# Kernel optimization log

Hardware: AMD Instinct MI355X
Metric: run time of the kernel (lower is better)

The kernel has to match this reference:

```python
import jax, jax.numpy as jnp
import numpy as np

S, B, D, H = 2048, 2, 1024, 16
DK = D // H  # 64

def setup_inputs() -> dict:
    key = jax.random.key(0)
    ks = jax.random.split(key, 11)
    scale = 1.0 / np.sqrt(D)
    return {
        "query": jax.random.normal(ks[0], (S, B, D), dtype=jnp.float32),
        "key":   jax.random.normal(ks[1], (S, B, D), dtype=jnp.float32),
        "value": jax.random.normal(ks[2], (S, B, D), dtype=jnp.float32),
        "Wq": jax.random.normal(ks[3], (D, D), dtype=jnp.float32) * scale,
        "bq": jax.random.normal(ks[4], (D,), dtype=jnp.float32) * scale,
        "Wk": jax.random.normal(ks[5], (D, D), dtype=jnp.float32) * scale,
        "bk": jax.random.normal(ks[6], (D,), dtype=jnp.float32) * scale,
        "Wv": jax.random.normal(ks[7], (D, D), dtype=jnp.float32) * scale,
        "bv": jax.random.normal(ks[8], (D,), dtype=jnp.float32) * scale,
        "Wo": jax.random.normal(ks[9], (D, D), dtype=jnp.float32) * scale,
        "bo": jax.random.normal(ks[10], (D,), dtype=jnp.float32) * scale,
    }

def _split_heads(x):
    # [S, B, D] -> [H, B, S, DK]  (matches .view(S,B,H,DK).transpose(0,2))
    return x.reshape(S, B, H, DK).transpose(2, 1, 0, 3)

def reference(query, key, value, Wq, bq, Wk, bk, Wv, bv, Wo, bo):
    q = _split_heads(query @ Wq.T + bq)
    k = _split_heads(key   @ Wk.T + bk)
    v = _split_heads(value @ Wv.T + bv)
    scores = jnp.einsum('hbqd,hbkd->hbqk', q, k) / jnp.sqrt(jnp.float32(DK))
    align = jax.nn.softmax(scores, axis=-1)
    x = jnp.einsum('hbqk,hbkd->hbqd', align, v)  # [H,B,S,DK]
    x = x.transpose(2, 1, 0, 3).reshape(S, B, D)  # back to [S,B,D]
    return x @ Wo.T + bo
```

## Files before the change

### kernel.cpp

```cpp
#include <hip/hip_runtime.h>
#include <math.h>

#define SS 2048
#define BB 2
#define DD 1024
#define HH 16
#define DKK 64
#define MM (SS*BB)

typedef _Float16 f16;
typedef __attribute__((ext_vector_type(8))) _Float16 f16x8;
typedef __attribute__((ext_vector_type(2))) __fp16 fp16x2r;
typedef __attribute__((ext_vector_type(4))) float f32x4;
typedef __attribute__((ext_vector_type(16))) float f32x16;

__device__ __forceinline__ unsigned pk2(float a, float b) {
    union { fp16x2r h; unsigned u; } v;
    v.h = __builtin_amdgcn_cvt_pkrtz(a, b);
    return v.u;
}
__device__ __forceinline__ void gload_lds16(const void* g, void* l) {
    __builtin_amdgcn_global_load_lds(
        (const __attribute__((address_space(1))) unsigned*)g,
        (__attribute__((address_space(3))) unsigned*)l, 16, 0, 0);
}

__global__ __launch_bounds__(256)
void cvt_x(const float* __restrict__ q, const float* __restrict__ k,
           const float* __restrict__ v, f16* __restrict__ out)
{
    const int z = blockIdx.y;
    const float* src = z == 0 ? q : (z == 1 ? k : v);
    size_t t = (size_t)blockIdx.x*256 + threadIdx.x;
    float4 f0 = ((const float4*)src)[t*2];
    float4 f1 = ((const float4*)src)[t*2+1];
    uint4 r;
    r.x = pk2(f0.x, f0.y); r.y = pk2(f0.z, f0.w);
    r.z = pk2(f1.x, f1.y); r.w = pk2(f1.z, f1.w);
    ((uint4*)(out + (size_t)z*MM*DD))[t] = r;
}

__global__ __launch_bounds__(256)
void cvt_w(const float* __restrict__ wq, const float* __restrict__ wk,
           const float* __restrict__ wv, const float* __restrict__ wo,
           f16* __restrict__ out)
{
    const int z = blockIdx.y;
    const float* src = z == 0 ? wq : (z == 1 ? wk : (z == 2 ? wv : wo));
    size_t t = (size_t)blockIdx.x*256 + threadIdx.x;
    float4 f0 = ((const float4*)src)[t*2];
    float4 f1 = ((const float4*)src)[t*2+1];
    uint4 r;
    r.x = pk2(f0.x, f0.y); r.y = pk2(f0.z, f0.w);
    r.z = pk2(f1.x, f1.y); r.w = pk2(f1.z, f1.w);
    ((uint4*)(out + (size_t)z*DD*DD))[t] = r;
}

__global__ __launch_bounds__(256)
void qkv_gemm(const f16* __restrict__ A16, const f16* __restrict__ W16,
              const float* __restrict__ bq, const float* __restrict__ bk,
              const float* __restrict__ bv,
              f16* __restrict__ Qh, f16* __restrict__ Kh, f16* __restrict__ Vt)
{
    __shared__ __align__(16) f16 As[128*32];
    __shared__ __align__(16) f16 Bs[128*32];

    const int tid  = threadIdx.x;
    const int w    = tid >> 6;
    const int lane = tid & 63;
    const int ln   = lane & 15;
    const int quad = lane >> 4;
    const int z  = blockIdx.z;
    const int m0 = blockIdx.x * 128;
    const int n0 = blockIdx.y * 128;
    const int wm = (w >> 1) * 64;
    const int wn = (w & 1) * 64;

    const f16* A = A16 + (size_t)z*MM*DD;
    const f16* W = W16 + (size_t)z*DD*DD;
    const float* bias = z == 0 ? bq : (z == 1 ? bk : bv);

    f32x4 acc[4][4];
    #pragma unroll
    for (int mt = 0; mt < 4; mt++)
        #pragma unroll
        for (int nt = 0; nt < 4; nt++)
            acc[mt][nt] = (f32x4){0.f,0.f,0.f,0.f};

    int slot[2], r_[2], gch[2];
    #pragma unroll
    for (int i = 0; i < 2; i++) {
        slot[i] = i*256 + tid;
        r_[i]   = slot[i] >> 2;
        gch[i]  = ((slot[i] & 3) ^ ((r_[i] >> 1) & 3)) * 8;
    }

    for (int step = 0; step < DD/32; step++) {
        const int k0 = step*32;
        __syncthreads();
        #pragma unroll
        for (int i = 0; i < 2; i++) {
            gload_lds16(A + (size_t)(m0 + r_[i])*DD + k0 + gch[i],
                        (char*)As + slot[i]*16);
            gload_lds16(W + (size_t)(n0 + r_[i])*DD + k0 + gch[i],
                        (char*)Bs + slot[i]*16);
        }
        __syncthreads();

        f16x8 af[4], bf[4];
        #pragma unroll
        for (int mt = 0; mt < 4; mt++) {
            int r = wm + mt*16 + ln;
            af[mt] = *(const f16x8*)&As[r*32 + ((quad ^ ((r>>1)&3)) << 3)];
        }
        #pragma unroll
        for (int nt = 0; nt < 4; nt++) {
            int r = wn + nt*16 + ln;
            bf[nt] = *(const f16x8*)&Bs[r*32 + ((quad ^ ((r>>1)&3)) << 3)];
        }
        #pragma unroll
        for (int mt = 0; mt < 4; mt++)
            #pragma unroll
            for (int nt = 0; nt < 4; nt++)
                acc[mt][nt] = __builtin_amdgcn_mfma_f32_16x16x32_f16(
                    af[mt], bf[nt], acc[mt][nt], 0, 0, 0);
    }

    float bvv[4];
    #pragma unroll
    for (int nt = 0; nt < 4; nt++) bvv[nt] = bias[n0 + wn + nt*16 + ln];

    if (z == 2) {
        #pragma unroll
        for (int mt = 0; mt < 4; mt++) {
            int mbase = m0 + wm + mt*16 + quad*4;
            int s0 = mbase >> 1;
            #pragma unroll
            for (int nt = 0; nt < 4; nt++) {
                int n = n0 + wn + nt*16 + ln;
                int h = n >> 6, d = n & 63;
                float v0 = acc[mt][nt][0] + bvv[nt];
                float v1 = acc[mt][nt][1] + bvv[nt];
                float v2 = acc[mt][nt][2] + bvv[nt];
                float v3 = acc[mt][nt][3] + bvv[nt];
                *(unsigned*)&Vt[((size_t)(0*HH + h)*DKK + d)*SS + s0] = pk2(v0, v2);
                *(unsigned*)&Vt[((size_t)(1*HH + h)*DKK + d)*SS + s0] = pk2(v1, v3);
            }
        }
    } else {
        const float scale = z == 0 ? 0.125f : 1.0f;
        f16* dst = z == 0 ? Qh : Kh;
        #pragma unroll
        for (int mt = 0; mt < 4; mt++)
            #pragma unroll
            for (int nt = 0; nt < 4; nt++)
                #pragma unroll
                for (int r = 0; r < 4; r++) {
                    int m = m0 + wm + mt*16 + quad*4 + r;
                    int n = n0 + wn + nt*16 + ln;
                    int s = m >> 1, b = m & 1;
                    int h = n >> 6, d = n & 63;
                    dst[(((size_t)(b*HH + h))*SS + s)*DKK + d] =
                        (f16)((acc[mt][nt][r] + bvv[nt]) * scale);
                }
    }
}

__global__ __launch_bounds__(256)
void out_gemm(const f16* __restrict__ A, const f16* __restrict__ W,
              const float* __restrict__ bias, float* __restrict__ out)
{
    __shared__ __align__(16) f16 As[64*32];
    __shared__ __align__(16) f16 Bs[128*32];

    const int tid  = threadIdx.x;
    const int w    = tid >> 6;
    const int lane = tid & 63;
    const int ln   = lane & 15;
    const int quad = lane >> 4;
    const int m0 = blockIdx.x * 64;
    const int n0 = blockIdx.y * 128;
    const int wm = (w >> 1) * 32;
    const int wn = (w & 1) * 64;

    f32x4 acc[2][4];
    #pragma unroll
    for (int mt = 0; mt < 2; mt++)
        #pragma unroll
        for (int nt = 0; nt < 4; nt++)
            acc[mt][nt] = (f32x4){0.f,0.f,0.f,0.f};

    const int rA  = tid >> 2;
    const int gchA = ((tid & 3) ^ ((rA >> 1) & 3)) * 8;
    int slotB[2], rB[2], gchB[2];
    #pragma unroll
    for (int i = 0; i < 2; i++) {
        slotB[i] = i*256 + tid;
        rB[i]    = slotB[i] >> 2;
        gchB[i]  = ((slotB[i] & 3) ^ ((rB[i] >> 1) & 3)) * 8;
    }

    for (int step = 0; step < DD/32; step++) {
        const int k0 = step*32;
        __syncthreads();
        gload_lds16(A + (size_t)(m0 + rA)*DD + k0 + gchA, (char*)As + tid*16);
        #pragma unroll
        for (int i = 0; i < 2; i++)
            gload_lds16(W + (size_t)(n0 + rB[i])*DD + k0 + gchB[i],
                        (char*)Bs + slotB[i]*16);
        __syncthreads();

        f16x8 af[2], bf[4];
        #pragma unroll
        for (int mt = 0; mt < 2; mt++) {
            int r = wm + mt*16 + ln;
            af[mt] = *(const f16x8*)&As[r*32 + ((quad ^ ((r>>1)&3)) << 3)];
        }
        #pragma unroll
        for (int nt = 0; nt < 4; nt++) {
            int r = wn + nt*16 + ln;
            bf[nt] = *(const f16x8*)&Bs[r*32 + ((quad ^ ((r>>1)&3)) << 3)];
        }
        #pragma unroll
        for (int mt = 0; mt < 2; mt++)
            #pragma unroll
            for (int nt = 0; nt < 4; nt++)
                acc[mt][nt] = __builtin_amdgcn_mfma_f32_16x16x32_f16(
                    af[mt], bf[nt], acc[mt][nt], 0, 0, 0);
    }

    #pragma unroll
    for (int nt = 0; nt < 4; nt++) {
        float bvv = bias[n0 + wn + nt*16 + ln];
        #pragma unroll
        for (int mt = 0; mt < 2; mt++)
            #pragma unroll
            for (int r = 0; r < 4; r++) {
                int m = m0 + wm + mt*16 + quad*4 + r;
                int n = n0 + wn + nt*16 + ln;
                out[(size_t)m*DD + n] = acc[mt][nt][r] + bvv;
            }
    }
}

__global__ __launch_bounds__(256)
void attn_v5(const f16* __restrict__ Q, const f16* __restrict__ K,
             const f16* __restrict__ V, f16* __restrict__ Xh)
{
    __shared__ __align__(16) f16 Ks[64*64];
    __shared__ __align__(16) f16 Vs[64*64];
    __shared__ __align__(16) f16 Pl[4*32*72];

    const int tid  = threadIdx.x;
    const int w    = tid >> 6;
    const int lane = tid & 63;
    const int l5   = lane & 31;
    const int hf   = lane >> 5;
    const int h = blockIdx.y, b = blockIdx.z;
    const size_t base = ((size_t)(b*HH + h)) * SS * DKK;
    const int Q0 = blockIdx.x * 128;

    f16x8 qf[4];
    #pragma unroll
    for (int ks = 0; ks < 4; ks++)
        qf[ks] = *(const f16x8*)(Q + base + (size_t)(Q0 + w*32 + l5)*DKK + ks*16 + hf*8);

    f16x8 ones;
    #pragma unroll
    for (int i = 0; i < 8; i++) ones[i] = (f16)1.0f;

    f32x16 o[2];
    o[0] = (f32x16)(0.f); o[1] = (f32x16)(0.f);
    f32x16 lacc = (f32x16)(0.f);

    const int slot0 = tid, slot1 = 256 + tid;
    const int sr0 = slot0 >> 3, sc0 = slot0 & 7;
    const int sr1 = slot1 >> 3, sc1 = slot1 & 7;
    f16* const myP = &Pl[w*2304 + l5*72];

    for (int kt = 0; kt < SS/64; kt++) {
        __syncthreads();
        gload_lds16(K + base + (size_t)(kt*64 + sr0)*DKK + ((sc0 ^ (sr0&7)) << 3),
                    (char*)Ks + slot0*16);
        gload_lds16(K + base + (size_t)(kt*64 + sr1)*DKK + ((sc1 ^ (sr1&7)) << 3),
                    (char*)Ks + slot1*16);
        gload_lds16(V + base + (size_t)sr0*SS + kt*64 + ((sc0 ^ (sr0&7)) << 3),
                    (char*)Vs + slot0*16);
        gload_lds16(V + base + (size_t)sr1*SS + kt*64 + ((sc1 ^ (sr1&7)) << 3),
                    (char*)Vs + slot1*16);
        __syncthreads();

        f32x16 sc[2];
        sc[0] = (f32x16)(0.f); sc[1] = (f32x16)(0.f);
        #pragma unroll
        for (int ks = 0; ks < 4; ks++) {
            const int cc = ks*2 + hf;
            #pragma unroll
            for (int mt = 0; mt < 2; mt++) {
                int key = mt*32 + l5;
                f16x8 ka = *(const f16x8*)&Ks[key*64 + ((cc ^ (key&7)) << 3)];
                sc[mt] = __builtin_amdgcn_mfma_f32_32x32x16_f16(ka, qf[ks], sc[mt], 0, 0, 0);
            }
        }

        #pragma unroll
        for (int mt = 0; mt < 2; mt++)
            #pragma unroll
            for (int g = 0; g < 4; g++) {
                float p0 = __expf(sc[mt][g*4+0]);
                float p1 = __expf(sc[mt][g*4+1]);
                float p2 = __expf(sc[mt][g*4+2]);
                float p3 = __expf(sc[mt][g*4+3]);
                uint2 pk;
                pk.x = pk2(p0, p1);
                pk.y = pk2(p2, p3);
                *(uint2*)&myP[mt*32 + g*8 + hf*4] = pk;
            }

        #pragma unroll
        for (int ks = 0; ks < 4; ks++) {
            f16x8 pb = *(const f16x8*)&myP[ks*16 + hf*8];
            lacc = __builtin_amdgcn_mfma_f32_32x32x16_f16(ones, pb, lacc, 0, 0, 0);
            const int cc = ks*2 + hf;
            #pragma unroll
            for (int mt = 0; mt < 2; mt++) {
                int d = mt*32 + l5;
                f16x8 va = *(const f16x8*)&Vs[d*64 + ((cc ^ (d&7)) << 3)];
                o[mt] = __builtin_amdgcn_mfma_f32_32x32x16_f16(va, pb, o[mt], 0, 0, 0);
            }
        }
    }

    const float inv = 1.0f / lacc[0];
    const int qg = Q0 + w*32 + l5;
    f16* xp = Xh + ((size_t)qg*BB + b)*DD + h*DKK;
    #pragma unroll
    for (int mt = 0; mt < 2; mt++)
        #pragma unroll
        for (int g = 0; g < 4; g++) {
            uint2 pk;
            pk.x = pk2(o[mt][g*4+0]*inv, o[mt][g*4+1]*inv);
            pk.y = pk2(o[mt][g*4+2]*inv, o[mt][g*4+3]*inv);
            *(uint2*)&xp[mt*32 + g*8 + hf*4] = pk;
        }
}

extern "C" void kernel_launch(void* const* d_in, const int* in_sizes, int n_in,
                              void* d_out, int out_size, void* d_ws, size_t ws_size,
                              hipStream_t stream) {
    (void)in_sizes; (void)n_in; (void)out_size; (void)ws_size;
    const float* query = (const float*)d_in[0];
    const float* key   = (const float*)d_in[1];
    const float* value = (const float*)d_in[2];
    const float* Wq = (const float*)d_in[3];
    const float* bq = (const float*)d_in[4];
    const float* Wk = (const float*)d_in[5];
    const float* bk = (const float*)d_in[6];
    const float* Wv = (const float*)d_in[7];
    const float* bv = (const float*)d_in[8];
    const float* Wo = (const float*)d_in[9];
    const float* bo = (const float*)d_in[10];

    char* ws = (char*)d_ws;
    f16* A16 = (f16*)ws;
    f16* W16 = (f16*)(ws + 25165824);
    f16* Qh  = (f16*)(ws + 33554432);
    f16* Kh  = (f16*)(ws + 41943040);
    f16* Vt  = (f16*)(ws + 50331648);
    f16* Xh  = (f16*)(ws + 58720256);

    cvt_x<<<dim3(MM*DD/8/256, 3), 256, 0, stream>>>(query, key, value, A16);
    cvt_w<<<dim3(DD*DD/8/256, 4), 256, 0, stream>>>(Wq, Wk, Wv, Wo, W16);

    qkv_gemm<<<dim3(MM/128, DD/128, 3), 256, 0, stream>>>(
        A16, W16, bq, bk, bv, Qh, Kh, Vt);

    attn_v5<<<dim3(SS/128, HH, BB), 256, 0, stream>>>(Qh, Kh, Vt, Xh);

    out_gemm<<<dim3(MM/64, DD/128), 256, 0, stream>>>(
        Xh, W16 + (size_t)3*DD*DD, bo, (float*)d_out);
}
```

Before: 229.8 us.

## Split attention key range across two wave groups and merge conversion kernels

After: 227.9 us. Within noise of the previous version (-0.8%).

```diff
diff --git a/kernel.cpp b/kernel.cpp
--- a/kernel.cpp
+++ b/kernel.cpp
@@ -26,34 +26,30 @@
 }
 
 __global__ __launch_bounds__(256)
-void cvt_x(const float* __restrict__ q, const float* __restrict__ k,
-           const float* __restrict__ v, f16* __restrict__ out)
+void cvt_all(const float* __restrict__ q, const float* __restrict__ k,
+             const float* __restrict__ v, const float* __restrict__ wq,
+             const float* __restrict__ wk, const float* __restrict__ wv,
+             const float* __restrict__ wo,
+             f16* __restrict__ xout, f16* __restrict__ wout)
 {
     const int z = blockIdx.y;
-    const float* src = z == 0 ? q : (z == 1 ? k : v);
+    const float* src;
+    f16* dst;
+    if (z < 3) {
+        src = z == 0 ? q : (z == 1 ? k : v);
+        dst = xout + (size_t)z*MM*DD;
+    } else {
+        if (blockIdx.x >= DD*DD/8/256) return;
+        src = z == 3 ? wq : (z == 4 ? wk : (z == 5 ? wv : wo));
+        dst = wout + (size_t)(z-3)*DD*DD;
+    }
     size_t t = (size_t)blockIdx.x*256 + threadIdx.x;
     float4 f0 = ((const float4*)src)[t*2];
     float4 f1 = ((const float4*)src)[t*2+1];
     uint4 r;
     r.x = pk2(f0.x, f0.y); r.y = pk2(f0.z, f0.w);
     r.z = pk2(f1.x, f1.y); r.w = pk2(f1.z, f1.w);
-    ((uint4*)(out + (size_t)z*MM*DD))[t] = r;
-}
-
-__global__ __launch_bounds__(256)
-void cvt_w(const float* __restrict__ wq, const float* __restrict__ wk,
-           const float* __restrict__ wv, const float* __restrict__ wo,
-           f16* __restrict__ out)
-{
-    const int z = blockIdx.y;
-    const float* src = z == 0 ? wq : (z == 1 ? wk : (z == 2 ? wv : wo));
-    size_t t = (size_t)blockIdx.x*256 + threadIdx.x;
-    float4 f0 = ((const float4*)src)[t*2];
-    float4 f1 = ((const float4*)src)[t*2+1];
-    uint4 r;
-    r.x = pk2(f0.x, f0.y); r.y = pk2(f0.z, f0.w);
-    r.z = pk2(f1.x, f1.y); r.w = pk2(f1.z, f1.w);
-    ((uint4*)(out + (size_t)z*DD*DD))[t] = r;
+    ((uint4*)dst)[t] = r;
 }
 
 __global__ __launch_bounds__(256)
@@ -243,27 +239,31 @@
     }
 }
 
-__global__ __launch_bounds__(256)
-void attn_v5(const f16* __restrict__ Q, const f16* __restrict__ K,
+__global__ __launch_bounds__(512, 4)
+void attn_v6(const f16* __restrict__ Q, const f16* __restrict__ K,
              const f16* __restrict__ V, f16* __restrict__ Xh)
 {
-    __shared__ __align__(16) f16 Ks[64*64];
-    __shared__ __align__(16) f16 Vs[64*64];
-    __shared__ __align__(16) f16 Pl[4*32*72];
+    __shared__ __align__(16) char arena[67584];
+    f16*   const PlBase = (f16*)(arena + 32768);
+    float* const Ol     = (float*)(arena + 32768);
+    float* const Ls     = (float*)(arena + 66048);
 
     const int tid  = threadIdx.x;
-    const int w    = tid >> 6;
+    const int g    = tid >> 8;
+    const int wg   = tid >> 6;
+    const int w4   = wg & 3;
     const int lane = tid & 63;
     const int l5   = lane & 31;
     const int hf   = lane >> 5;
     const int h = blockIdx.y, b = blockIdx.z;
     const size_t base = ((size_t)(b*HH + h)) * SS * DKK;
     const int Q0 = blockIdx.x * 128;
+    const int q  = w4*32 + l5;
 
     f16x8 qf[4];
     #pragma unroll
     for (int ks = 0; ks < 4; ks++)
-        qf[ks] = *(const f16x8*)(Q + base + (size_t)(Q0 + w*32 + l5)*DKK + ks*16 + hf*8);
+        qf[ks] = *(const f16x8*)(Q + base + (size_t)(Q0 + q)*DKK + ks*16 + hf*8);
 
     f16x8 ones;
     #pragma unroll
@@ -273,21 +273,25 @@
     o[0] = (f32x16)(0.f); o[1] = (f32x16)(0.f);
     f32x16 lacc = (f32x16)(0.f);
 
-    const int slot0 = tid, slot1 = 256 + tid;
-    const int sr0 = slot0 >> 3, sc0 = slot0 & 7;
-    const int sr1 = slot1 >> 3, sc1 = slot1 & 7;
-    f16* const myP = &Pl[w*2304 + l5*72];
-
-    for (int kt = 0; kt < SS/64; kt++) {
-        __syncthreads();
-        gload_lds16(K + base + (size_t)(kt*64 + sr0)*DKK + ((sc0 ^ (sr0&7)) << 3),
-                    (char*)Ks + slot0*16);
-        gload_lds16(K + base + (size_t)(kt*64 + sr1)*DKK + ((sc1 ^ (sr1&7)) << 3),
-                    (char*)Ks + slot1*16);
-        gload_lds16(V + base + (size_t)sr0*SS + kt*64 + ((sc0 ^ (sr0&7)) << 3),
-                    (char*)Vs + slot0*16);
-        gload_lds16(V + base + (size_t)sr1*SS + kt*64 + ((sc1 ^ (sr1&7)) << 3),
-                    (char*)Vs + slot1*16);
+    const f16* const Ksg = (const f16*)(arena + g*8192);
+    const f16* const Vsg = (const f16*)(arena + 16384 + g*8192);
+    f16* const myP = PlBase + wg*2176 + l5*68;
+
+    for (int t = 0; t < 16; t++) {
+        __syncthreads();
+        #pragma unroll
+        for (int i = 0; i < 4; i++) {
+            int slot = i*512 + tid;
+            int kv   = slot >> 10;
+            int s    = (slot >> 9) & 1;
+            int idx  = slot & 511;
+            int r    = idx >> 3, c8 = idx & 7;
+            int kts  = s*16 + t;
+            const f16* src = kv == 0
+                ? K + base + (size_t)(kts*64 + r)*DKK + ((c8 ^ (r&7)) << 3)
+                : V + base + (size_t)r*SS + kts*64 + ((c8 ^ (r&7)) << 3);
+            gload_lds16(src, arena + kv*16384 + s*8192 + idx*16);
+        }
         __syncthreads();
 
         f32x16 sc[2];
@@ -298,7 +302,7 @@
             #pragma unroll
             for (int mt = 0; mt < 2; mt++) {
                 int key = mt*32 + l5;
-                f16x8 ka = *(const f16x8*)&Ks[key*64 + ((cc ^ (key&7)) << 3)];
+                f16x8 ka = *(const f16x8*)&Ksg[key*64 + ((cc ^ (key&7)) << 3)];
                 sc[mt] = __builtin_amdgcn_mfma_f32_32x32x16_f16(ka, qf[ks], sc[mt], 0, 0, 0);
             }
         }
@@ -306,43 +310,60 @@
         #pragma unroll
         for (int mt = 0; mt < 2; mt++)
             #pragma unroll
-            for (int g = 0; g < 4; g++) {
-                float p0 = __expf(sc[mt][g*4+0]);
-                float p1 = __expf(sc[mt][g*4+1]);
-                float p2 = __expf(sc[mt][g*4+2]);
-                float p3 = __expf(sc[mt][g*4+3]);
+            for (int gg = 0; gg < 4; gg++) {
                 uint2 pk;
-                pk.x = pk2(p0, p1);
-                pk.y = pk2(p2, p3);
-                *(uint2*)&myP[mt*32 + g*8 + hf*4] = pk;
+                pk.x = pk2(__expf(sc[mt][gg*4+0]), __expf(sc[mt][gg*4+1]));
+                pk.y = pk2(__expf(sc[mt][gg*4+2]), __expf(sc[mt][gg*4+3]));
+                *(uint2*)&myP[mt*32 + gg*8 + hf*4] = pk;
             }
 
         #pragma unroll
         for (int ks = 0; ks < 4; ks++) {
-            f16x8 pb = *(const f16x8*)&myP[ks*16 + hf*8];
+            union { uint2 u[2]; f16x8 v; } pbu;
+            pbu.u[0] = *(const uint2*)&myP[ks*16 + hf*8];
+            pbu.u[1] = *(const uint2*)&myP[ks*16 + hf*8 + 4];
+            f16x8 pb = pbu.v;
             lacc = __builtin_amdgcn_mfma_f32_32x32x16_f16(ones, pb, lacc, 0, 0, 0);
             const int cc = ks*2 + hf;
             #pragma unroll
             for (int mt = 0; mt < 2; mt++) {
                 int d = mt*32 + l5;
-                f16x8 va = *(const f16x8*)&Vs[d*64 + ((cc ^ (d&7)) << 3)];
+                f16x8 va = *(const f16x8*)&Vsg[d*64 + ((cc ^ (d&7)) << 3)];
                 o[mt] = __builtin_amdgcn_mfma_f32_32x32x16_f16(va, pb, o[mt], 0, 0, 0);
             }
         }
     }
 
-    const float inv = 1.0f / lacc[0];
-    const int qg = Q0 + w*32 + l5;
-    f16* xp = Xh + ((size_t)qg*BB + b)*DD + h*DKK;
-    #pragma unroll
-    for (int mt = 0; mt < 2; mt++)
-        #pragma unroll
-        for (int g = 0; g < 4; g++) {
-            uint2 pk;
-            pk.x = pk2(o[mt][g*4+0]*inv, o[mt][g*4+1]*inv);
-            pk.y = pk2(o[mt][g*4+2]*inv, o[mt][g*4+3]*inv);
-            *(uint2*)&xp[mt*32 + g*8 + hf*4] = pk;
-        }
+    __syncthreads();
+    if (g == 1) {
+        #pragma unroll
+        for (int mt = 0; mt < 2; mt++)
+            #pragma unroll
+            for (int reg = 0; reg < 16; reg++) {
+                int d = mt*32 + (reg & 3) + 8*(reg >> 2) + 4*hf;
+                Ol[q*65 + d] = o[mt][reg];
+            }
+        if (hf == 0) Ls[q] = lacc[0];
+    }
+    __syncthreads();
+    if (g == 0) {
+        const float inv = 1.0f / (lacc[0] + Ls[q]);
+        const int qg = Q0 + q;
+        f16* xp = Xh + ((size_t)qg*BB + b)*DD + h*DKK;
+        #pragma unroll
+        for (int mt = 0; mt < 2; mt++)
+            #pragma unroll
+            for (int gg = 0; gg < 4; gg++) {
+                float v0 = (o[mt][gg*4+0] + Ol[q*65 + mt*32 + 8*gg + 4*hf + 0]) * inv;
+                float v1 = (o[mt][gg*4+1] + Ol[q*65 + mt*32 + 8*gg + 4*hf + 1]) * inv;
+                float v2 = (o[mt][gg*4+2] + Ol[q*65 + mt*32 + 8*gg + 4*hf + 2]) * inv;
+                float v3 = (o[mt][gg*4+3] + Ol[q*65 + mt*32 + 8*gg + 4*hf + 3]) * inv;
+                uint2 pk;
+                pk.x = pk2(v0, v1);
+                pk.y = pk2(v2, v3);
+                *(uint2*)&xp[mt*32 + gg*8 + hf*4] = pk;
+            }
+    }
 }
 
 extern "C" void kernel_launch(void* const* d_in, const int* in_sizes, int n_in,
@@ -369,13 +390,13 @@
     f16* Vt  = (f16*)(ws + 50331648);
     f16* Xh  = (f16*)(ws + 58720256);
 
-    cvt_x<<<dim3(MM*DD/8/256, 3), 256, 0, stream>>>(query, key, value, A16);
-    cvt_w<<<dim3(DD*DD/8/256, 4), 256, 0, stream>>>(Wq, Wk, Wv, Wo, W16);
+    cvt_all<<<dim3(MM*DD/8/256, 7), 256, 0, stream>>>(
+        query, key, value, Wq, Wk, Wv, Wo, A16, W16);
 
     qkv_gemm<<<dim3(MM/128, DD/128, 3), 256, 0, stream>>>(
         A16, W16, bq, bk, bv, Qh, Kh, Vt);
 
-    attn_v5<<<dim3(SS/128, HH, BB), 256, 0, stream>>>(Qh, Kh, Vt, Xh);
+    attn_v6<<<dim3(SS/128, HH, BB), 512, 0, stream>>>(Qh, Kh, Vt, Xh);
 
     out_gemm<<<dim3(MM/64, DD/128), 256, 0, stream>>>(
         Xh, W16 + (size_t)3*DD*DD, bo, (float*)d_out);
```
